# Optimization experiments

Measured on AMD Instinct MI355X. Metric: run time of the kernel, lower is better.

Reference implementation:

```python
import jax, jax.numpy as jnp
import numpy as np
from jax import lax

BN_EPS = 1e-5


def _conv_block(x, w, b):
    # conv k=3 pad=1 (NCHW), relu, maxpool 2x2 stride 2 (floor)
    y = lax.conv_general_dilated(x, w, (1, 1), [(1, 1), (1, 1)],
                                 dimension_numbers=('NCHW', 'OIHW', 'NCHW'))
    y = jax.nn.relu(y + b[None, :, None, None])
    y = lax.reduce_window(y, -jnp.inf, lax.max, (1, 1, 2, 2), (1, 1, 2, 2), 'VALID')
    return y


def _batchnorm_train(x, g, b):
    # BatchNorm2d in train mode: biased batch stats over (N,H,W)
    m = jnp.mean(x, axis=(0, 2, 3), keepdims=True)
    v = jnp.mean(jnp.square(x - m), axis=(0, 2, 3), keepdims=True)
    return g[None, :, None, None] * (x - m) * lax.rsqrt(v + BN_EPS) + b[None, :, None, None]


def setup_inputs() -> dict:
    key = jax.random.key(0)
    ks = jax.random.split(key, 16)
    B = 4096
    s = lambda k, shape, fan: jax.random.normal(k, shape, jnp.float32) * (1.0 / np.sqrt(fan))
    return {
        'x':   jax.random.normal(ks[0], (B, 1, 28, 28), jnp.float32),
        'cw1': s(ks[1], (32, 1, 3, 3), 9),    'cb1': jnp.zeros((32,), jnp.float32),
        'cw2': s(ks[2], (32, 32, 3, 3), 288), 'cb2': jnp.zeros((32,), jnp.float32),
        'cw3': s(ks[3], (32, 32, 3, 3), 288), 'cb3': jnp.zeros((32,), jnp.float32),
        'bn_g': jnp.ones((32,), jnp.float32), 'bn_b': jnp.zeros((32,), jnp.float32),
        'pw1': s(ks[4], (288, 128), 288), 'pb1': jnp.zeros((128,), jnp.float32),
        'pw2': s(ks[5], (128, 128), 128), 'pb2': jnp.zeros((128,), jnp.float32),
        'pw3': s(ks[6], (128, 3), 128),   'pb3': jnp.zeros((3,), jnp.float32),
        'ew1': s(ks[7], (3, 288, 128), 288), 'eb1': jnp.zeros((3, 128), jnp.float32),
        'ew2': s(ks[8], (3, 128, 128), 128), 'eb2': jnp.zeros((3, 128), jnp.float32),
        'ew3': s(ks[9], (3, 128, 10), 128),  'eb3': jnp.zeros((3, 10), jnp.float32),
    }


def _select_linear(h, oh, ew, eb):
    # per-example expert Linear: compute all 3 tiny experts, pick via one-hot
    y = jnp.einsum('bi,eio->beo', h, ew) + eb[None]  # [B,3,out]
    return jnp.einsum('beo,be->bo', y, oh)


def reference(x, cw1, cb1, cw2, cb2, cw3, cb3, bn_g, bn_b,
              pw1, pb1, pw2, pb2, pw3, pb3,
              ew1, eb1, ew2, eb2, ew3, eb3):
    # conv stack
    y = _conv_block(x, cw1, cb1)
    y = _conv_block(y, cw2, cb2)
    y = _conv_block(y, cw3, cb3)
    y = _batchnorm_train(y, bn_g, bn_b)
    y = y.reshape(y.shape[0], -1)  # [B, 288]

    # ActorCritic approx policy MLP (288 -> 128 -> 128 -> 3), greedy action
    h = jax.nn.relu(y @ pw1 + pb1)
    h = jax.nn.relu(h @ pw2 + pb2)
    logits = h @ pw3 + pb3
    actions = jnp.argmax(logits, axis=-1)          # [B] int, routing decision
    oh = jax.nn.one_hot(actions, 3, dtype=y.dtype)  # [B,3]

    # three SelectionLayers, same per-example routing decision
    y = _select_linear(y, oh, ew1, eb1)
    y = _select_linear(y, oh, ew2, eb2)
    y = _select_linear(y, oh, ew3, eb3)  # [B,10]
    return y, actions
```

## Files before the change

kernel.cpp:

```cpp
#include <hip/hip_runtime.h>

__global__ __launch_bounds__(256) void repack_kernel(
    const float* __restrict__ cw2, const float* __restrict__ cw3,
    float* __restrict__ packed2, float* __restrict__ packed3)
{
    int t = blockIdx.x * 256 + threadIdx.x;
    if (t < 9216) {
        int oc = t & 31, r = t >> 5;
        packed2[t] = cw2[oc * 288 + r];
    } else {
        int t2 = t - 9216;
        int oc = t2 & 31, r = t2 >> 5;
        packed3[t2] = cw3[oc * 288 + r];
    }
}

__global__ __launch_bounds__(256)
void fused_conv_kernel(
    const float* __restrict__ x,
    const float* __restrict__ cw1, const float* __restrict__ cb1,
    const float* __restrict__ packed2, const float* __restrict__ cb2,
    const float* __restrict__ packed3, const float* __restrict__ cb3,
    float* __restrict__ out3, float* __restrict__ gstats)
{
    const int img = blockIdx.x;
    const int tid = threadIdx.x;

    __shared__ float A[1220];
    __shared__ float B[8320];
    __shared__ float b2s[32], b3s[32];

    float* xs1  = A;
    float* w1s  = A + 900;
    float* b1s  = A + 1188;
    float* wck2 = A;
    float* xs2  = B;
    float* sc   = B;
    float* xs3  = B + 1280;
    float* wck3 = B + 4160;
    float* sc2  = B + 5073;

    for (int i = tid; i < 900;  i += 256) xs1[i] = 0.f;
    for (int i = tid; i < 8320; i += 256) B[i] = 0.f;
    __syncthreads();

    for (int i = tid; i < 784; i += 256) {
        int yy = i / 28, xx = i % 28;
        xs1[(yy + 1) * 30 + xx + 1] = x[img * 784 + i];
    }
    for (int i = tid; i < 288; i += 256) {
        int oc = i & 31, tap = i >> 5;
        w1s[i] = cw1[oc * 9 + tap];
    }
    if (tid < 32) { b1s[tid] = cb1[tid]; b2s[tid] = cb2[tid]; b3s[tid] = cb3[tid]; }
    __syncthreads();

    {
        const int c1 = tid & 31;
        float w1r[9];
        #pragma unroll
        for (int t = 0; t < 9; t++) w1r[t] = w1s[t * 32 + c1];
        const float bias1 = b1s[c1];
        for (int o = tid; o < 32 * 196; o += 256) {
            int p = o >> 5;
            int py = p / 14, px = p % 14;
            int base = (2 * py) * 30 + 2 * px;
            float P[16];
            #pragma unroll
            for (int r = 0; r < 4; r++) {
                float2 u0 = *(const float2*)&xs1[base + r * 30];
                float2 u1 = *(const float2*)&xs1[base + r * 30 + 2];
                P[r * 4 + 0] = u0.x; P[r * 4 + 1] = u0.y;
                P[r * 4 + 2] = u1.x; P[r * 4 + 3] = u1.y;
            }
            float a00 = 0.f, a01 = 0.f, a10 = 0.f, a11 = 0.f;
            #pragma unroll
            for (int ky = 0; ky < 3; ky++)
                #pragma unroll
                for (int kx = 0; kx < 3; kx++) {
                    float w = w1r[ky * 3 + kx];
                    a00 = fmaf(P[ky * 4 + kx],           w, a00);
                    a01 = fmaf(P[ky * 4 + kx + 1],       w, a01);
                    a10 = fmaf(P[(ky + 1) * 4 + kx],     w, a10);
                    a11 = fmaf(P[(ky + 1) * 4 + kx + 1], w, a11);
                }
            float v = fmaxf(fmaxf(fmaxf(a00, a01), fmaxf(a10, a11)) + bias1, 0.f);
            int r = py + 1, col = px + 1;
            xs2[c1 * 260 + r * 16 + ((((col >> 2) + r) & 3) << 2) + (col & 3)] = v;
        }
    }

    const int g  = tid >> 7;
    const int u  = tid & 127;
    const int cb = u & 7, R = u >> 3;
    const int oc0 = cb * 4;
    const bool act2 = (u < 112);

    float acc[4][14];
    #pragma unroll
    for (int a = 0; a < 4; a++)
        #pragma unroll
        for (int c = 0; c < 14; c++) acc[a][c] = 0.f;

    float pf[5];
    #pragma unroll
    for (int k = 0; k < 5; k++) {
        int idx = tid + k * 256;
        pf[k] = (idx < 1152) ? packed2[idx] : 0.f;
    }

    for (int ch = 0; ch < 8; ch++) {
        __syncthreads();
        #pragma unroll
        for (int k = 0; k < 5; k++) {
            int idx = tid + k * 256;
            if (idx < 1152) wck2[idx] = pf[k];
        }
        if (ch < 7) {
            #pragma unroll
            for (int k = 0; k < 5; k++) {
                int idx = tid + k * 256;
                pf[k] = (idx < 1152) ? packed2[(ch + 1) * 1152 + idx] : 0.f;
            }
        }
        __syncthreads();
        if (act2) {
            #pragma unroll
            for (int d = 0; d < 2; d++) {
                const int ld = g * 2 + d;
                const int ic = ch * 4 + ld;
                const float* wd = &wck2[ld * 288 + oc0];
                const int pb = ic * 260;
                #pragma unroll
                for (int ky = 0; ky < 3; ky++) {
                    const int rp = R + ky;
                    const int rb = pb + rp * 16;
                    float row[16];
                    #pragma unroll
                    for (int q = 0; q < 4; q++) {
                        const float4 t = *(const float4*)&xs2[rb + (((q + rp) & 3) << 2)];
                        row[q * 4 + 0] = t.x; row[q * 4 + 1] = t.y;
                        row[q * 4 + 2] = t.z; row[q * 4 + 3] = t.w;
                    }
                    const float4 wa = *(const float4*)&wd[(ky * 3 + 0) * 32];
                    const float4 wb = *(const float4*)&wd[(ky * 3 + 1) * 32];
                    const float4 wc = *(const float4*)&wd[(ky * 3 + 2) * 32];
                    #pragma unroll
                    for (int c = 0; c < 14; c++) {
                        acc[0][c] = fmaf(row[c],     wa.x, acc[0][c]);
                        acc[1][c] = fmaf(row[c],     wa.y, acc[1][c]);
                        acc[2][c] = fmaf(row[c],     wa.z, acc[2][c]);
                        acc[3][c] = fmaf(row[c],     wa.w, acc[3][c]);
                        acc[0][c] = fmaf(row[c + 1], wb.x, acc[0][c]);
                        acc[1][c] = fmaf(row[c + 1], wb.y, acc[1][c]);
                        acc[2][c] = fmaf(row[c + 1], wb.z, acc[2][c]);
                        acc[3][c] = fmaf(row[c + 1], wb.w, acc[3][c]);
                        acc[0][c] = fmaf(row[c + 2], wc.x, acc[0][c]);
                        acc[1][c] = fmaf(row[c + 2], wc.y, acc[1][c]);
                        acc[2][c] = fmaf(row[c + 2], wc.z, acc[2][c]);
                        acc[3][c] = fmaf(row[c + 2], wc.w, acc[3][c]);
                    }
                }
            }
        }
    }

    __syncthreads();
    if (g == 1 && act2) {
        #pragma unroll
        for (int a = 0; a < 4; a++)
            #pragma unroll
            for (int c = 0; c < 14; c++) sc[u * 57 + a * 14 + c] = acc[a][c];
    }
    __syncthreads();
    if (g == 0 && act2) {
        #pragma unroll
        for (int a = 0; a < 4; a++)
            #pragma unroll
            for (int c = 0; c < 14; c++) acc[a][c] += sc[u * 57 + a * 14 + c];
    }
    __syncthreads();

    for (int i = tid; i < 2880; i += 256) xs3[i] = 0.f;
    float hm[4][7];
    if (g == 0 && act2) {
        #pragma unroll
        for (int a = 0; a < 4; a++)
            #pragma unroll
            for (int c = 0; c < 7; c++)
                hm[a][c] = fmaxf(acc[a][2 * c], acc[a][2 * c + 1]);
        if (R & 1) {
            #pragma unroll
            for (int a = 0; a < 4; a++)
                #pragma unroll
                for (int c = 0; c < 7; c++) sc2[u * 29 + a * 7 + c] = hm[a][c];
        }
    }
    __syncthreads();
    if (g == 0 && act2 && !(R & 1)) {
        const int py = R >> 1;
        #pragma unroll
        for (int a = 0; a < 4; a++)
            #pragma unroll
            for (int c = 0; c < 7; c++) {
                float v = fmaxf(hm[a][c], sc2[(u + 8) * 29 + a * 7 + c]);
                v = fmaxf(v + b2s[oc0 + a], 0.f);
                xs3[(oc0 + a) * 90 + (py + 1) * 10 + (c + 1)] = v;
            }
    }

    const int u3 = tid & 127;
    const bool act3 = (u3 < 72);
    const int cq3 = u3 & 7, pos = u3 >> 3;
    const int oc30 = cq3 * 4;
    const int py3 = pos / 3, px3 = pos % 3;
    const int base3 = (2 * py3) * 10 + 2 * px3;

    float a3[4][4];
    #pragma unroll
    for (int a = 0; a < 4; a++)
        #pragma unroll
        for (int q = 0; q < 4; q++) a3[a][q] = 0.f;

    float pg[9];
    #pragma unroll
    for (int k = 0; k < 9; k++) pg[k] = packed3[tid + k * 256];

    for (int ch = 0; ch < 4; ch++) {
        __syncthreads();
        #pragma unroll
        for (int k = 0; k < 9; k++) wck3[tid + k * 256] = pg[k];
        if (ch < 3) {
            #pragma unroll
            for (int k = 0; k < 9; k++) pg[k] = packed3[(ch + 1) * 2304 + tid + k * 256];
        }
        __syncthreads();
        if (act3) {
            #pragma unroll 2
            for (int d = 0; d < 4; d++) {
                const int ld = g * 4 + d;
                const int ic = ch * 8 + ld;
                const float* xp = &xs3[ic * 90 + base3];
                float P[16];
                #pragma unroll
                for (int r = 0; r < 4; r++) {
                    float2 u0 = *(const float2*)&xp[r * 10];
                    float2 u1 = *(const float2*)&xp[r * 10 + 2];
                    P[r * 4 + 0] = u0.x; P[r * 4 + 1] = u0.y;
                    P[r * 4 + 2] = u1.x; P[r * 4 + 3] = u1.y;
                }
                const float* wd = &wck3[ld * 288 + oc30];
                #pragma unroll
                for (int tap = 0; tap < 9; tap++) {
                    const int ky = tap / 3, kx = tap % 3;
                    const float4 wv = *(const float4*)&wd[tap * 32];
                    const float x00 = P[ky * 4 + kx];
                    const float x01 = P[ky * 4 + kx + 1];
                    const float x10 = P[(ky + 1) * 4 + kx];
                    const float x11 = P[(ky + 1) * 4 + kx + 1];
                    a3[0][0] = fmaf(x00, wv.x, a3[0][0]); a3[0][1] = fmaf(x01, wv.x, a3[0][1]);
                    a3[0][2] = fmaf(x10, wv.x, a3[0][2]); a3[0][3] = fmaf(x11, wv.x, a3[0][3]);
                    a3[1][0] = fmaf(x00, wv.y, a3[1][0]); a3[1][1] = fmaf(x01, wv.y, a3[1][1]);
                    a3[1][2] = fmaf(x10, wv.y, a3[1][2]); a3[1][3] = fmaf(x11, wv.y, a3[1][3]);
                    a3[2][0] = fmaf(x00, wv.z, a3[2][0]); a3[2][1] = fmaf(x01, wv.z, a3[2][1]);
                    a3[2][2] = fmaf(x10, wv.z, a3[2][2]); a3[2][3] = fmaf(x11, wv.z, a3[2][3]);
                    a3[3][0] = fmaf(x00, wv.w, a3[3][0]); a3[3][1] = fmaf(x01, wv.w, a3[3][1]);
                    a3[3][2] = fmaf(x10, wv.w, a3[3][2]); a3[3][3] = fmaf(x11, wv.w, a3[3][3]);
                }
            }
        }
    }

    __syncthreads();
    if (g == 1 && act3) {
        #pragma unroll
        for (int a = 0; a < 4; a++)
            #pragma unroll
            for (int q = 0; q < 4; q++) sc[u3 * 17 + a * 4 + q] = a3[a][q];
    }
    __syncthreads();
    float rres[4];
    const bool writer = (g == 0 && act3);
    if (writer) {
        #pragma unroll
        for (int a = 0; a < 4; a++)
            #pragma unroll
            for (int q = 0; q < 4; q++) a3[a][q] += sc[u3 * 17 + a * 4 + q];
        float4 res;
        #pragma unroll
        for (int a = 0; a < 4; a++) {
            float v = fmaxf(fmaxf(a3[a][0], a3[a][1]), fmaxf(a3[a][2], a3[a][3]));
            rres[a] = fmaxf(v + b3s[oc30 + a], 0.f);
        }
        res.x = rres[0]; res.y = rres[1]; res.z = rres[2]; res.w = rres[3];
        *(float4*)&out3[img * 288 + pos * 32 + oc30] = res;
    }

    __syncthreads();
    for (int i = tid; i < 576; i += 256) B[i] = 0.f;
    __syncthreads();
    if (writer) {
        #pragma unroll
        for (int a = 0; a < 4; a++) {
            B[pos * 64 + oc30 + a]      = rres[a];
            B[pos * 64 + 32 + oc30 + a] = rres[a] * rres[a];
        }
    }
    __syncthreads();
    if (tid < 64) {
        int c = tid & 31, part = tid >> 5;
        float s = 0.f;
        #pragma unroll
        for (int p = 0; p < 9; p++) s += B[p * 64 + part * 32 + c];
        atomicAdd(&gstats[part * 32 + c], s);
    }
}

__global__ __launch_bounds__(512) void mlp_select_kernel(
    const float* __restrict__ out3, const float* __restrict__ gstats,
    const float* __restrict__ bng, const float* __restrict__ bnb,
    const float* __restrict__ pw1, const float* __restrict__ pb1,
    const float* __restrict__ pw2, const float* __restrict__ pb2,
    const float* __restrict__ pw3, const float* __restrict__ pb3,
    const float* __restrict__ ew1, const float* __restrict__ eb1,
    const float* __restrict__ ew2, const float* __restrict__ eb2,
    const float* __restrict__ ew3, const float* __restrict__ eb3,
    float* __restrict__ out)
{
    const int tid = threadIdx.x;
    const int img0 = blockIdx.x * 8;

    __shared__ float ysT[288 * 14];
    __shared__ float hAT[128 * 14];
    __shared__ float hBT[128 * 14];
    __shared__ float wst[32 * 128];
    __shared__ float lgp[48];
    __shared__ float sp[160];
    __shared__ int   acts[8];
    __shared__ float sa[32], sb[32];

    if (tid < 32) {
        float S = gstats[tid], SS = gstats[32 + tid];
        const float inv_n = 1.f / (4096.f * 9.f);
        float mean = S * inv_n;
        float var = SS * inv_n - mean * mean;
        float a = bng[tid] * rsqrtf(var + 1e-5f);
        sa[tid] = a;
        sb[tid] = bnb[tid] - a * mean;
    }
    __syncthreads();

    for (int it = 0; it < 2; it++) {
        int i4 = it * 512 + tid;
        if (i4 < 576) {
            int e = i4 / 72, jq = i4 - e * 72;
            float4 v = *(const float4*)&out3[(img0 + e) * 288 + jq * 4];
            int j = jq * 4;
            ysT[(j + 0) * 14 + e] = fmaf(sa[(j + 0) & 31], v.x, sb[(j + 0) & 31]);
            ysT[(j + 1) * 14 + e] = fmaf(sa[(j + 1) & 31], v.y, sb[(j + 1) & 31]);
            ysT[(j + 2) * 14 + e] = fmaf(sa[(j + 2) & 31], v.z, sb[(j + 2) & 31]);
            ysT[(j + 3) * 14 + e] = fmaf(sa[(j + 3) & 31], v.w, sb[(j + 3) & 31]);
        }
    }

    const int kg = tid >> 8;
    const int t8 = tid & 255;
    const int n4 = t8 & 31;
    const int eE = t8 >> 5;
    const int j0 = kg * 16;
    float acc[4];

    {
        acc[0] = 0.f; acc[1] = 0.f; acc[2] = 0.f; acc[3] = 0.f;
        for (int t = 0; t < 9; t++) {
            __syncthreads();
            #pragma unroll
            for (int s = 0; s < 2; s++) {
                int idx = s * 512 + tid;
                int row = idx >> 5, c4 = idx & 31;
                int k = t * 32 + row;
                int i = (k & 31) * 9 + (k >> 5);
                *(float4*)&wst[row * 128 + c4 * 4] =
                    *(const float4*)&pw1[i * 128 + c4 * 4];
            }
            __syncthreads();
            #pragma unroll
            for (int j = 0; j < 16; j++) {
                float4 w = *(const float4*)&wst[(j0 + j) * 128 + n4 * 4];
                float yv = ysT[(t * 32 + j0 + j) * 14 + eE];
                acc[0] = fmaf(yv, w.x, acc[0]); acc[1] = fmaf(yv, w.y, acc[1]);
                acc[2] = fmaf(yv, w.z, acc[2]); acc[3] = fmaf(yv, w.w, acc[3]);
            }
        }
        __syncthreads();
        if (kg) *(float4*)&wst[t8 * 4] = make_float4(acc[0], acc[1], acc[2], acc[3]);
        __syncthreads();
        if (!kg) {
            float4 p = *(const float4*)&wst[t8 * 4];
            float4 b = *(const float4*)&pb1[n4 * 4];
            hAT[(n4 * 4 + 0) * 14 + eE] = fmaxf(acc[0] + p.x + b.x, 0.f);
            hAT[(n4 * 4 + 1) * 14 + eE] = fmaxf(acc[1] + p.y + b.y, 0.f);
            hAT[(n4 * 4 + 2) * 14 + eE] = fmaxf(acc[2] + p.z + b.z, 0.f);
            hAT[(n4 * 4 + 3) * 14 + eE] = fmaxf(acc[3] + p.w + b.w, 0.f);
        }
    }

    {
        acc[0] = 0.f; acc[1] = 0.f; acc[2] = 0.f; acc[3] = 0.f;
        for (int t = 0; t < 4; t++) {
            __syncthreads();
            #pragma unroll
            for (int s = 0; s < 2; s++) {
                int idx = s * 512 + tid;
                int row = idx >> 5, c4 = idx & 31;
                int k = t * 32 + row;
                *(float4*)&wst[row * 128 + c4 * 4] =
                    *(const float4*)&pw2[k * 128 + c4 * 4];
            }
            __syncthreads();
            #pragma unroll
            for (int j = 0; j < 16; j++) {
                float4 w = *(const float4*)&wst[(j0 + j) * 128 + n4 * 4];
                float hv = hAT[(t * 32 + j0 + j) * 14 + eE];
                acc[0] = fmaf(hv, w.x, acc[0]); acc[1] = fmaf(hv, w.y, acc[1]);
                acc[2] = fmaf(hv, w.z, acc[2]); acc[3] = fmaf(hv, w.w, acc[3]);
            }
        }
        __syncthreads();
        if (kg) *(float4*)&wst[t8 * 4] = make_float4(acc[0], acc[1], acc[2], acc[3]);
        __syncthreads();
        if (!kg) {
            float4 p = *(const float4*)&wst[t8 * 4];
            float4 b = *(const float4*)&pb2[n4 * 4];
            hBT[(n4 * 4 + 0) * 14 + eE] = fmaxf(acc[0] + p.x + b.x, 0.f);
            hBT[(n4 * 4 + 1) * 14 + eE] = fmaxf(acc[1] + p.y + b.y, 0.f);
            hBT[(n4 * 4 + 2) * 14 + eE] = fmaxf(acc[2] + p.z + b.z, 0.f);
            hBT[(n4 * 4 + 3) * 14 + eE] = fmaxf(acc[3] + p.w + b.w, 0.f);
        }
    }
    __syncthreads();

    if (tid < 48) {
        int pr = tid & 1, eo = tid >> 1;
        int e = eo / 3, o = eo - e * 3;
        float s = pr ? 0.f : pb3[o];
        const int k0 = pr * 64;
        for (int k = k0; k < k0 + 64; k++) s = fmaf(hBT[k * 14 + e], pw3[k * 3 + o], s);
        lgp[tid] = s;
    }
    __syncthreads();
    if (tid < 8) {
        float l0 = lgp[(tid * 3 + 0) * 2] + lgp[(tid * 3 + 0) * 2 + 1];
        float l1 = lgp[(tid * 3 + 1) * 2] + lgp[(tid * 3 + 1) * 2 + 1];
        float l2 = lgp[(tid * 3 + 2) * 2] + lgp[(tid * 3 + 2) * 2 + 1];
        int a = 0; float best = l0;
        if (l1 > best) { best = l1; a = 1; }
        if (l2 > best) { best = l2; a = 2; }
        acts[tid] = a;
        out[4096 * 10 + img0 + tid] = (float)a;
    }
    __syncthreads();

    const int a = acts[eE];

    {
        const float* wb = ew1 + a * 36864;
        acc[0] = 0.f; acc[1] = 0.f; acc[2] = 0.f; acc[3] = 0.f;
        const int kb = kg * 144;
        for (int kk = 0; kk < 144; kk++) {
            int k = kb + kk;
            int i = (k & 31) * 9 + (k >> 5);
            float4 w = *(const float4*)&wb[i * 128 + n4 * 4];
            float yv = ysT[k * 14 + eE];
            acc[0] = fmaf(yv, w.x, acc[0]); acc[1] = fmaf(yv, w.y, acc[1]);
            acc[2] = fmaf(yv, w.z, acc[2]); acc[3] = fmaf(yv, w.w, acc[3]);
        }
        __syncthreads();
        if (kg) *(float4*)&wst[t8 * 4] = make_float4(acc[0], acc[1], acc[2], acc[3]);
        __syncthreads();
        if (!kg) {
            float4 p = *(const float4*)&wst[t8 * 4];
            float4 b = *(const float4*)&eb1[a * 128 + n4 * 4];
            hAT[(n4 * 4 + 0) * 14 + eE] = acc[0] + p.x + b.x;
            hAT[(n4 * 4 + 1) * 14 + eE] = acc[1] + p.y + b.y;
            hAT[(n4 * 4 + 2) * 14 + eE] = acc[2] + p.z + b.z;
            hAT[(n4 * 4 + 3) * 14 + eE] = acc[3] + p.w + b.w;
        }
    }
    __syncthreads();

    {
        const float* wb = ew2 + a * 16384;
        acc[0] = 0.f; acc[1] = 0.f; acc[2] = 0.f; acc[3] = 0.f;
        const int kb = kg * 64;
        for (int kk = 0; kk < 64; kk++) {
            int k = kb + kk;
            float4 w = *(const float4*)&wb[k * 128 + n4 * 4];
            float hv = hAT[k * 14 + eE];
            acc[0] = fmaf(hv, w.x, acc[0]); acc[1] = fmaf(hv, w.y, acc[1]);
            acc[2] = fmaf(hv, w.z, acc[2]); acc[3] = fmaf(hv, w.w, acc[3]);
        }
        __syncthreads();
        if (kg) *(float4*)&wst[t8 * 4] = make_float4(acc[0], acc[1], acc[2], acc[3]);
        __syncthreads();
        if (!kg) {
            float4 p = *(const float4*)&wst[t8 * 4];
            float4 b = *(const float4*)&eb2[a * 128 + n4 * 4];
            hBT[(n4 * 4 + 0) * 14 + eE] = acc[0] + p.x + b.x;
            hBT[(n4 * 4 + 1) * 14 + eE] = acc[1] + p.y + b.y;
            hBT[(n4 * 4 + 2) * 14 + eE] = acc[2] + p.z + b.z;
            hBT[(n4 * 4 + 3) * 14 + eE] = acc[3] + p.w + b.w;
        }
    }
    __syncthreads();

    if (tid < 160) {
        int pr = (tid >= 80) ? 1 : 0;
        int idx = tid - pr * 80;
        int e = idx / 10, o = idx - e * 10;
        int aa = acts[e];
        const float* w3 = &ew3[aa * 1280];
        float s = pr ? 0.f : eb3[aa * 10 + o];
        const int k0 = pr * 64;
        for (int k = k0; k < k0 + 64; k++) s = fmaf(hBT[k * 14 + e], w3[k * 10 + o], s);
        sp[tid] = s;
    }
    __syncthreads();
    if (tid < 80) {
        int e = tid / 10, o = tid - e * 10;
        out[(img0 + e) * 10 + o] = sp[tid] + sp[tid + 80];
    }
}

extern "C" void kernel_launch(void* const* d_in, const int* in_sizes, int n_in,
                              void* d_out, int out_size, void* d_ws, size_t ws_size,
                              hipStream_t stream)
{
    const float* x   = (const float*)d_in[0];
    const float* cw1 = (const float*)d_in[1];
    const float* cb1 = (const float*)d_in[2];
    const float* cw2 = (const float*)d_in[3];
    const float* cb2 = (const float*)d_in[4];
    const float* cw3 = (const float*)d_in[5];
    const float* cb3 = (const float*)d_in[6];
    const float* bng = (const float*)d_in[7];
    const float* bnb = (const float*)d_in[8];
    const float* pw1 = (const float*)d_in[9];
    const float* pb1 = (const float*)d_in[10];
    const float* pw2 = (const float*)d_in[11];
    const float* pb2 = (const float*)d_in[12];
    const float* pw3 = (const float*)d_in[13];
    const float* pb3 = (const float*)d_in[14];
    const float* ew1 = (const float*)d_in[15];
    const float* eb1 = (const float*)d_in[16];
    const float* ew2 = (const float*)d_in[17];
    const float* eb2 = (const float*)d_in[18];
    const float* ew3 = (const float*)d_in[19];
    const float* eb3 = (const float*)d_in[20];

    float* out     = (float*)d_out;
    float* out3    = (float*)d_ws;
    float* gstats  = out3 + 4096 * 288;
    float* packed2 = gstats + 64;
    float* packed3 = packed2 + 9216;

    hipMemsetAsync(gstats, 0, 64 * sizeof(float), stream);
    repack_kernel<<<72, 256, 0, stream>>>(cw2, cw3, packed2, packed3);
    fused_conv_kernel<<<4096, 256, 0, stream>>>(x, cw1, cb1, packed2, cb2,
                                                packed3, cb3, out3, gstats);
    mlp_select_kernel<<<512, 512, 0, stream>>>(out3, gstats, bng, bnb,
                                               pw1, pb1, pw2, pb2, pw3, pb3,
                                               ew1, eb1, ew2, eb2, ew3, eb3, out);
}
```

Before: 413.0 us.

## Stage expert weights through shared memory with register prefetch double-buffering

The expert Linear layers used to read per-thread weights straight from global memory, with a separate row chosen per example's action. Now all three experts' weight tiles (16 rows) are loaded cooperatively into shared memory and each thread picks its action's slice from there. The next tile is prefetched into registers while the current one is consumed, and the first ew1 and ew2 tiles are issued early to hide latency. This adds 24KB of shared memory, which may lower occupancy, plus extra barriers, and it loads all three experts even though only the selected ones are used.

```diff
diff --git a/kernel.cpp b/kernel.cpp
--- a/kernel.cpp
+++ b/kernel.cpp
@@ -334,6 +334,7 @@
     __shared__ float hAT[128 * 14];
     __shared__ float hBT[128 * 14];
     __shared__ float wst[32 * 128];
+    __shared__ float west[3 * 16 * 128];
     __shared__ float lgp[48];
     __shared__ float sp[160];
     __shared__ int   acts[8];
@@ -368,6 +369,8 @@
     const int n4 = t8 & 31;
     const int eE = t8 >> 5;
     const int j0 = kg * 16;
+    const int srow16 = tid >> 5;
+    const int sc4b   = tid & 31;
     float acc[4];
 
     {
@@ -439,6 +442,14 @@
         }
     }
     __syncthreads();
+
+    float4 pfe[3];
+    {
+        const int i0 = (srow16 & 31) * 9 + (srow16 >> 5);
+        #pragma unroll
+        for (int s = 0; s < 3; s++)
+            pfe[s] = *(const float4*)&ew1[s * 36864 + i0 * 128 + sc4b * 4];
+    }
 
     if (tid < 48) {
         int pr = tid & 1, eo = tid >> 1;
@@ -464,17 +475,32 @@
     const int a = acts[eE];
 
     {
-        const float* wb = ew1 + a * 36864;
         acc[0] = 0.f; acc[1] = 0.f; acc[2] = 0.f; acc[3] = 0.f;
-        const int kb = kg * 144;
-        for (int kk = 0; kk < 144; kk++) {
-            int k = kb + kk;
-            int i = (k & 31) * 9 + (k >> 5);
-            float4 w = *(const float4*)&wb[i * 128 + n4 * 4];
-            float yv = ysT[k * 14 + eE];
-            acc[0] = fmaf(yv, w.x, acc[0]); acc[1] = fmaf(yv, w.y, acc[1]);
-            acc[2] = fmaf(yv, w.z, acc[2]); acc[3] = fmaf(yv, w.w, acc[3]);
-        }
+        for (int t = 0; t < 18; t++) {
+            __syncthreads();
+            #pragma unroll
+            for (int s = 0; s < 3; s++)
+                *(float4*)&west[s * 2048 + srow16 * 128 + sc4b * 4] = pfe[s];
+            if (t < 17) {
+                int k = (t + 1) * 16 + srow16;
+                int i = (k & 31) * 9 + (k >> 5);
+                #pragma unroll
+                for (int s = 0; s < 3; s++)
+                    pfe[s] = *(const float4*)&ew1[s * 36864 + i * 128 + sc4b * 4];
+            }
+            __syncthreads();
+            #pragma unroll
+            for (int j = 0; j < 8; j++) {
+                int kr = kg * 8 + j;
+                float4 w = *(const float4*)&west[a * 2048 + kr * 128 + n4 * 4];
+                float yv = ysT[(t * 16 + kr) * 14 + eE];
+                acc[0] = fmaf(yv, w.x, acc[0]); acc[1] = fmaf(yv, w.y, acc[1]);
+                acc[2] = fmaf(yv, w.z, acc[2]); acc[3] = fmaf(yv, w.w, acc[3]);
+            }
+        }
+        #pragma unroll
+        for (int s = 0; s < 3; s++)
+            pfe[s] = *(const float4*)&ew2[s * 16384 + srow16 * 128 + sc4b * 4];
         __syncthreads();
         if (kg) *(float4*)&wst[t8 * 4] = make_float4(acc[0], acc[1], acc[2], acc[3]);
         __syncthreads();
@@ -487,18 +513,29 @@
             hAT[(n4 * 4 + 3) * 14 + eE] = acc[3] + p.w + b.w;
         }
     }
-    __syncthreads();
 
     {
-        const float* wb = ew2 + a * 16384;
         acc[0] = 0.f; acc[1] = 0.f; acc[2] = 0.f; acc[3] = 0.f;
-        const int kb = kg * 64;
-        for (int kk = 0; kk < 64; kk++) {
-            int k = kb + kk;
-            float4 w = *(const float4*)&wb[k * 128 + n4 * 4];
-            float hv = hAT[k * 14 + eE];
-            acc[0] = fmaf(hv, w.x, acc[0]); acc[1] = fmaf(hv, w.y, acc[1]);
-            acc[2] = fmaf(hv, w.z, acc[2]); acc[3] = fmaf(hv, w.w, acc[3]);
+        for (int t = 0; t < 8; t++) {
+            __syncthreads();
+            #pragma unroll
+            for (int s = 0; s < 3; s++)
+                *(float4*)&west[s * 2048 + srow16 * 128 + sc4b * 4] = pfe[s];
+            if (t < 7) {
+                int k = (t + 1) * 16 + srow16;
+                #pragma unroll
+                for (int s = 0; s < 3; s++)
+                    pfe[s] = *(const float4*)&ew2[s * 16384 + k * 128 + sc4b * 4];
+            }
+            __syncthreads();
+            #pragma unroll
+            for (int j = 0; j < 8; j++) {
+                int kr = kg * 8 + j;
+                float4 w = *(const float4*)&west[a * 2048 + kr * 128 + n4 * 4];
+                float hv = hAT[(t * 16 + kr) * 14 + eE];
+                acc[0] = fmaf(hv, w.x, acc[0]); acc[1] = fmaf(hv, w.y, acc[1]);
+                acc[2] = fmaf(hv, w.z, acc[2]); acc[3] = fmaf(hv, w.w, acc[3]);
+            }
         }
         __syncthreads();
         if (kg) *(float4*)&wst[t8 * 4] = make_float4(acc[0], acc[1], acc[2], acc[3]);
```

Result: slower. 478.3 us (+15.8%).
